# Optimization experiments

Measured on AMD Instinct MI355X. Metric: run time of the kernel, lower is better.

The kernel has to match this reference:

```python
import jax, jax.numpy as jnp
import numpy as np

IGNORE = 0  # ignore label (default in LovaszSoftmax.__init__)


def setup_inputs() -> dict:
    key = jax.random.key(0)
    k1, k2 = jax.random.split(key)
    B, C, H, W = 4, 20, 512, 1024
    logits = jax.random.normal(k1, (B, C, H, W), dtype=jnp.float32)
    labels = jax.random.randint(k2, (B, H, W), 0, 20, dtype=jnp.int32)
    return {"logits": logits, "labels": labels}


def _lovasz_softmax(logits, labels, ignore=IGNORE):
    # logits: [B,C,H,W], labels: [B,H,W]
    B, C, H, W = logits.shape
    probas = jax.nn.softmax(logits, axis=1)
    pf = probas.transpose(0, 2, 3, 1).reshape(-1, C)  # [N, C]
    lf = labels.reshape(-1)                            # [N]
    valid = lf != ignore                               # [N]

    def per_class(c):
        # Ignored pixels get fg=0 and pred=0 -> error 0, so they sort to the
        # tail and contribute 0 to the dot product (equivalent to filtering
        # them out, but jit-compatible with static shapes).
        fg = ((lf == c) & valid).astype(pf.dtype)      # [N]
        pred = jnp.where(valid, pf[:, c], 0.0)         # [N]
        errors = jnp.abs(fg - pred)
        order = jnp.argsort(-errors)                   # descending sort perm
        errors_sorted = errors[order]
        fg_sorted = fg[order]
        # Lovasz gradient of sorted ground truth
        gts = fg_sorted.sum()
        intersection = gts - jnp.cumsum(fg_sorted)
        union = gts + jnp.cumsum(1.0 - fg_sorted)
        jaccard = 1.0 - intersection / union
        jaccard = jnp.concatenate([jaccard[:1], jaccard[1:] - jaccard[:-1]])
        loss_c = jnp.dot(errors_sorted, jaccard)
        present = fg.sum() > 0                          # classes='present'
        return loss_c, present

    losses, present = jax.vmap(per_class)(jnp.arange(C))
    p = present.astype(losses.dtype)
    # mean over present classes (matches 'present' + mean() in torch source)
    return jnp.sum(losses * p) / jnp.maximum(jnp.sum(p), 1.0)


def reference(logits, labels):
    return _lovasz_softmax(logits, labels, IGNORE)
```

## Files before the change

kernel.cpp:

```cpp
#include <hip/hip_runtime.h>

#define NCLS 20
#define NBIN 192
#define RREP 4
#define HWSZ (512*1024)
#define NPIX (4*HWSZ)
#define NBLK 512
#define NTHR 1024

__global__ __launch_bounds__(NTHR)
void hist_kernel(const float* __restrict__ logits,
                 const int* __restrict__ labels,
                 unsigned int* __restrict__ bhist)
{
    __shared__ unsigned int lh[NCLS * NBIN * RREP];
    for (int i = threadIdx.x; i < NCLS * NBIN * RREP; i += NTHR) lh[i] = 0u;
    __syncthreads();

    const int tid = blockIdx.x * NTHR + threadIdx.x;
    const int r = threadIdx.x & (RREP - 1);

    for (int n = tid; n < NPIX; n += NBLK * NTHR) {
        const int b  = n >> 19;
        const int hw = n & (HWSZ - 1);
        const float* base = logits + (size_t)b * NCLS * HWSZ + hw;

        float x[NCLS];
        float m = -1e30f;
#pragma unroll
        for (int c = 0; c < NCLS; c++) {
            x[c] = base[(size_t)c * HWSZ];
            m = fmaxf(m, x[c]);
        }
        float Z = 0.f;
#pragma unroll
        for (int c = 0; c < NCLS; c++) {
            x[c] = __expf(x[c] - m);
            Z += x[c];
        }
        const float invZ = 1.f / Z;

        const int lbl = labels[n];
        const bool valid = (lbl != 0);

#pragma unroll
        for (int c = 0; c < NCLS; c++) {
            const float p = x[c] * invZ;
            const bool fg = valid && (lbl == c);
            const float e = valid ? (fg ? 1.f - p : p) : 0.f;
            int bin = (int)(e * (float)NBIN);
            bin = bin > (NBIN - 1) ? (NBIN - 1) : bin;
            atomicAdd(&lh[(c * NBIN + bin) * RREP + r], fg ? 0x10001u : 1u);
        }
    }
    __syncthreads();

    unsigned int* out = bhist + (size_t)blockIdx.x * (NCLS * NBIN);
    for (int i = threadIdx.x; i < NCLS * NBIN; i += NTHR) {
        out[i] = lh[i * RREP + 0] + lh[i * RREP + 1] +
                 lh[i * RREP + 2] + lh[i * RREP + 3];
    }
}

__global__ void scan_kernel(const unsigned int* __restrict__ bhist,
                            float* __restrict__ cls)
{
    __shared__ float scnt[NBIN];
    __shared__ float sfg[NBIN];
    const int c = blockIdx.x;
    const int t = threadIdx.x;

    unsigned int cnt = 0, fg = 0;
    for (int b = 0; b < NBLK; b++) {
        const unsigned int v = bhist[(size_t)b * (NCLS * NBIN) + c * NBIN + t];
        cnt += v & 0xFFFFu;
        fg  += v >> 16;
    }
    scnt[t] = (float)cnt;
    sfg[t]  = (float)fg;
    __syncthreads();

    if (t < 64) {
        const int lane = t;
        float fgsum = 0.f;
        for (int j = lane; j < NBIN; j += 64) fgsum += sfg[j];
        for (int off = 32; off; off >>= 1) fgsum += __shfl_down(fgsum, off);
        const float gts = __shfl(fgsum, 0);

        float loss = 0.f;
        if (gts > 0.f) {
            float Tc = 0.f, Fc = 0.f;
            float acc = 0.f;
            for (int chunk = 0; chunk < NBIN / 64; chunk++) {
                const int k = NBIN - 1 - (chunk * 64 + lane);
                float ci = scnt[k];
                float fi = sfg[k];
                const float cnt_k = ci, fg_k = fi;
                for (int off = 1; off < 64; off <<= 1) {
                    const float cu = __shfl_up(ci, off);
                    const float fu = __shfl_up(fi, off);
                    if (lane >= off) { ci += cu; fi += fu; }
                }
                const float T1 = Tc + ci, F1 = Fc + fi;
                const float T0 = T1 - cnt_k, F0 = F1 - fg_k;

                const float J1 = 1.f - (gts - F1) / (gts + T1 - F1);
                const float J0 = 1.f - (gts - F0) / (gts + T0 - F0);
                const float center = ((float)k + 0.5f) * (1.0f / (float)NBIN);
                acc += center * (J1 - J0);

                Tc = __shfl(T1, 63);
                Fc = __shfl(F1, 63);
            }
            for (int off = 32; off; off >>= 1) acc += __shfl_down(acc, off);
            loss = acc;
        }
        if (lane == 0) {
            cls[c]        = loss;
            cls[NCLS + c] = (gts > 0.f) ? 1.f : 0.f;
        }
    }
}

__global__ void finalize_kernel(const float* __restrict__ cls,
                                float* __restrict__ out)
{
    if (threadIdx.x == 0 && blockIdx.x == 0) {
        float sl = 0.f, sp = 0.f;
        for (int c = 0; c < NCLS; c++) {
            sl += cls[c] * cls[NCLS + c];
            sp += cls[NCLS + c];
        }
        out[0] = sl / fmaxf(sp, 1.f);
    }
}

extern "C" void kernel_launch(void* const* d_in, const int* in_sizes, int n_in,
                              void* d_out, int out_size, void* d_ws, size_t ws_size,
                              hipStream_t stream)
{
    const float* logits = (const float*)d_in[0];
    const int*   labels = (const int*)d_in[1];

    unsigned int* bhist = (unsigned int*)d_ws;
    float* cls = (float*)((char*)d_ws + (size_t)NBLK * NCLS * NBIN * 4);

    hist_kernel<<<NBLK, NTHR, 0, stream>>>(logits, labels, bhist);
    scan_kernel<<<NCLS, NBIN, 0, stream>>>(bhist, cls);
    finalize_kernel<<<1, 1, 0, stream>>>(cls, (float*)d_out);
}
```

Measured before the change: 266.0 us.

## Process two pixels per thread, skip bin-0 non-fg atomics, parallelize scan reduction

The histogram kernel now handles two adjacent pixels per thread with float2/int2 loads, fully unrolled over a fixed two iterations. It merges atomics when both pixels land in the same bin and skips atomics for non-foreground entries in bin 0. The scan kernel reconstructs the skipped bin-0 count from the total pixel count. The scan kernel also splits the per-block histogram reduction across four thread groups. This cuts LDS atomic traffic and the serial scan latency, but the hardcoded iteration count ties the kernel to the exact problem size.

```diff
diff --git a/kernel.cpp b/kernel.cpp
--- a/kernel.cpp
+++ b/kernel.cpp
@@ -7,8 +7,9 @@
 #define NPIX (4*HWSZ)
 #define NBLK 512
 #define NTHR 1024
+#define SGRP 4
 
-__global__ __launch_bounds__(NTHR)
+__global__ __launch_bounds__(NTHR, 4)
 void hist_kernel(const float* __restrict__ logits,
                  const int* __restrict__ labels,
                  unsigned int* __restrict__ bhist)
@@ -17,40 +18,56 @@
     for (int i = threadIdx.x; i < NCLS * NBIN * RREP; i += NTHR) lh[i] = 0u;
     __syncthreads();
 
-    const int tid = blockIdx.x * NTHR + threadIdx.x;
     const int r = threadIdx.x & (RREP - 1);
 
-    for (int n = tid; n < NPIX; n += NBLK * NTHR) {
+#pragma unroll
+    for (int iter = 0; iter < 2; iter++) {
+        const int pp = (iter * NBLK + blockIdx.x) * NTHR + threadIdx.x;
+        const int n  = pp << 1;
         const int b  = n >> 19;
         const int hw = n & (HWSZ - 1);
-        const float* base = logits + (size_t)b * NCLS * HWSZ + hw;
+        const float2* base =
+            (const float2*)(logits + (size_t)b * NCLS * HWSZ + hw);
 
-        float x[NCLS];
-        float m = -1e30f;
+        float2 x[NCLS];
+        float m0 = -1e30f, m1 = -1e30f;
 #pragma unroll
         for (int c = 0; c < NCLS; c++) {
-            x[c] = base[(size_t)c * HWSZ];
-            m = fmaxf(m, x[c]);
+            x[c] = base[c * (HWSZ / 2)];
+            m0 = fmaxf(m0, x[c].x);
+            m1 = fmaxf(m1, x[c].y);
         }
-        float Z = 0.f;
+        float Z0 = 0.f, Z1 = 0.f;
 #pragma unroll
         for (int c = 0; c < NCLS; c++) {
-            x[c] = __expf(x[c] - m);
-            Z += x[c];
+            x[c].x = __expf(x[c].x - m0);
+            x[c].y = __expf(x[c].y - m1);
+            Z0 += x[c].x;
+            Z1 += x[c].y;
         }
-        const float invZ = 1.f / Z;
+        const float invZ0 = 1.f / Z0;
+        const float invZ1 = 1.f / Z1;
 
-        const int lbl = labels[n];
-        const bool valid = (lbl != 0);
+        const int2 lv = ((const int2*)labels)[pp];
+        const bool v0 = (lv.x != 0), v1 = (lv.y != 0);
 
 #pragma unroll
         for (int c = 0; c < NCLS; c++) {
-            const float p = x[c] * invZ;
-            const bool fg = valid && (lbl == c);
-            const float e = valid ? (fg ? 1.f - p : p) : 0.f;
-            int bin = (int)(e * (float)NBIN);
-            bin = bin > (NBIN - 1) ? (NBIN - 1) : bin;
-            atomicAdd(&lh[(c * NBIN + bin) * RREP + r], fg ? 0x10001u : 1u);
+            const float p0 = x[c].x * invZ0;
+            const float p1 = x[c].y * invZ1;
+            const bool f0 = v0 && (lv.x == c);
+            const bool f1 = v1 && (lv.y == c);
+            const float e0 = v0 ? (f0 ? 1.f - p0 : p0) : 0.f;
+            const float e1 = v1 ? (f1 ? 1.f - p1 : p1) : 0.f;
+            int b0 = (int)(e0 * (float)NBIN); b0 = b0 > NBIN-1 ? NBIN-1 : b0;
+            int b1 = (int)(e1 * (float)NBIN); b1 = b1 > NBIN-1 ? NBIN-1 : b1;
+            unsigned q0 = f0 ? 0x10001u : 1u;
+            unsigned q1 = f1 ? 0x10001u : 1u;
+            if (b0 == b1) { q0 += q1; q1 = 0u; }
+            if (!(b0 == 0 && q0 < 0x10000u))
+                atomicAdd(&lh[(c * NBIN + b0) * RREP + r], q0);
+            if (q1 && !(b1 == 0 && q1 < 0x10000u))
+                atomicAdd(&lh[(c * NBIN + b1) * RREP + r], q1);
         }
     }
     __syncthreads();
@@ -65,19 +82,41 @@
 __global__ void scan_kernel(const unsigned int* __restrict__ bhist,
                             float* __restrict__ cls)
 {
+    __shared__ float pcnt[SGRP][NBIN];
+    __shared__ float pfg[SGRP][NBIN];
     __shared__ float scnt[NBIN];
     __shared__ float sfg[NBIN];
+    __shared__ float stot;
+
     const int c = blockIdx.x;
     const int t = threadIdx.x;
+    const int g = t / NBIN;
+    const int bin = t - g * NBIN;
 
     unsigned int cnt = 0, fg = 0;
-    for (int b = 0; b < NBLK; b++) {
-        const unsigned int v = bhist[(size_t)b * (NCLS * NBIN) + c * NBIN + t];
+    for (int b = g * (NBLK / SGRP); b < (g + 1) * (NBLK / SGRP); b++) {
+        const unsigned int v = bhist[(size_t)b * (NCLS * NBIN) + c * NBIN + bin];
         cnt += v & 0xFFFFu;
         fg  += v >> 16;
     }
-    scnt[t] = (float)cnt;
-    sfg[t]  = (float)fg;
+    pcnt[g][bin] = (float)cnt;
+    pfg[g][bin]  = (float)fg;
+    __syncthreads();
+
+    if (t < NBIN) {
+        scnt[t] = pcnt[0][t] + pcnt[1][t] + pcnt[2][t] + pcnt[3][t];
+        sfg[t]  = pfg[0][t]  + pfg[1][t]  + pfg[2][t]  + pfg[3][t];
+    }
+    __syncthreads();
+
+    if (t < 64) {
+        float tot = 0.f;
+        for (int j = t; j < NBIN; j += 64) tot += scnt[j];
+        for (int off = 32; off; off >>= 1) tot += __shfl_down(tot, off);
+        if (t == 0) stot = tot;
+    }
+    __syncthreads();
+    if (t == 0) scnt[0] += (float)NPIX - stot;
     __syncthreads();
 
     if (t < 64) {
@@ -89,8 +128,7 @@
 
         float loss = 0.f;
         if (gts > 0.f) {
-            float Tc = 0.f, Fc = 0.f;
-            float acc = 0.f;
+            float Tc = 0.f, Fc = 0.f, acc = 0.f;
             for (int chunk = 0; chunk < NBIN / 64; chunk++) {
                 const int k = NBIN - 1 - (chunk * 64 + lane);
                 float ci = scnt[k];
@@ -146,6 +184,6 @@
     float* cls = (float*)((char*)d_ws + (size_t)NBLK * NCLS * NBIN * 4);
 
     hist_kernel<<<NBLK, NTHR, 0, stream>>>(logits, labels, bhist);
-    scan_kernel<<<NCLS, NBIN, 0, stream>>>(bhist, cls);
+    scan_kernel<<<NCLS, SGRP * NBIN, 0, stream>>>(bhist, cls);
     finalize_kernel<<<1, 1, 0, stream>>>(cls, (float*)d_out);
 }
```

New measurement: 257.3 us. -3.3%, faster.
